# Kernel tuning notes

Hardware: AMD Instinct MI355X
Metric: run time of the kernel (lower is better)

## Reference

```python
import jax, jax.numpy as jnp
from jax import lax
import numpy as np

THRESHOLD = 0.9
KHALF = 5  # conv_kernel_size; full conv width = 2*KHALF + 1 = 11


def _cif_scan(eouts, alpha_norm, elens, ylens, Lp1):
    """Vectorized-over-batch integrate-and-fire scan over time (lax.scan)."""
    B, T, D = eouts.shape
    bidx = jnp.arange(B)
    dt = eouts.dtype

    def step(carry, xs):
        alpha_accum, state, n_tok, fired = carry
        a_t, e_t, t = xs  # a_t: [B], e_t: [B,D], t: scalar int
        alpha_accum = alpha_accum + a_t
        active = (t <= elens - 1) & (n_tok < ylens)
        fire = active & (alpha_accum >= THRESHOLD)
        ak1 = 1.0 - alpha_accum
        ak2 = a_t - ak1
        # attention-weight column for time t
        aw_col = jnp.zeros((B, Lp1), dt)
        w_old = jnp.where(fire, ak1, jnp.where(active, a_t, jnp.zeros((), dt)))
        aw_col = aw_col.at[bidx, n_tok].add(w_old)
        n_new = n_tok + fire.astype(n_tok.dtype)
        aw_col = aw_col.at[bidx, n_new].add(jnp.where(fire, ak2, jnp.zeros((), dt)))
        # fired output row (set once per token slot)
        fire_val = state + ak1[:, None] * e_t
        cur = fired[bidx, n_tok]
        fired = fired.at[bidx, n_tok].set(jnp.where(fire[:, None], fire_val, cur))
        # integrate / reset state
        state = jnp.where(fire[:, None], ak2[:, None] * e_t,
                          jnp.where(active[:, None], state + a_t[:, None] * e_t, state))
        alpha_accum = jnp.where(fire, ak2, alpha_accum)
        return (alpha_accum, state, n_new, fired), aw_col

    init = (jnp.zeros((B,), dt), jnp.zeros((B, D), dt),
            jnp.zeros((B,), jnp.int32), jnp.zeros((B, Lp1, D), dt))
    xs = (jnp.swapaxes(alpha_norm, 0, 1), jnp.swapaxes(eouts, 0, 1),
          jnp.arange(T))
    (_, _, _, fired), aw_cols = lax.scan(step, init, xs)
    aws = jnp.transpose(aw_cols, (1, 2, 0))[:, None]  # [B,1,Lp1,T]
    return fired, aws


def _forward(eouts, conv_w, conv_b, proj_w, proj_b, elens, ylens, L):
    # Conv1d over time, 'same' padding: [B,T,D] -> [B,T,C]
    conv_feat = lax.conv_general_dilated(
        eouts, conv_w, window_strides=(1,), padding=[(KHALF, KHALF)],
        dimension_numbers=('NWC', 'WIO', 'NWC')) + conv_b
    alpha = jax.nn.sigmoid(conv_feat @ proj_w + proj_b)[:, :, 0]  # [B,T]
    alpha_norm = alpha / jnp.sum(alpha, axis=1, keepdims=True) \
        * ylens[:, None].astype(alpha.dtype)
    fired, aws = _cif_scan(eouts, alpha_norm, elens, ylens, L + 1)
    return fired[:, :L], alpha, aws


def setup_inputs():
    key = jax.random.key(0)
    k1, k2, k3, k4, k5 = jax.random.split(key, 5)
    B, T, D, C = 16, 2048, 512, 512
    eouts = jax.random.normal(k1, (B, T, D), jnp.float32)
    elens = jnp.maximum(jax.random.randint(k2, (B,), 0, T), T // 2).astype(jnp.int32)
    ylens = jnp.maximum(jax.random.randint(k3, (B,), 0, 128), 32).astype(jnp.int32)
    conv_w = jax.random.normal(k4, (2 * KHALF + 1, D, C), jnp.float32) * 0.02
    conv_b = jnp.zeros((C,), jnp.float32)
    proj_w = jax.random.normal(k5, (C, 1), jnp.float32) * 0.05
    proj_b = jnp.zeros((1,), jnp.float32)
    return dict(eouts=eouts, conv_w=conv_w, conv_b=conv_b,
                proj_w=proj_w, proj_b=proj_b, elens=elens, ylens=ylens)


def reference(eouts, conv_w, conv_b, proj_w, proj_b, elens, ylens):
    L = int(jnp.max(ylens))  # max_len = ylens.max(), as in the original
    return _forward(eouts, conv_w, conv_b, proj_w, proj_b, elens, ylens, L)
```

## Files before the change

### kernel.cpp

```cpp
#include <hip/hip_runtime.h>
#include <math.h>

#define KHALF 5
#define MAXF 256

__global__ void k_weff(const float* __restrict__ conv_w, const float* __restrict__ conv_b,
                       const float* __restrict__ proj_w, const float* __restrict__ proj_b,
                       float* __restrict__ w_eff, float* __restrict__ b_eff,
                       int KD, int C) {
    int gid = blockIdx.x * blockDim.x + threadIdx.x;
    int wave = gid >> 6;
    int lane = gid & 63;
    if (wave > KD) return;
    float s = 0.f;
    if (wave < KD) {
        const float* row = conv_w + (size_t)wave * C;
        for (int c = lane * 4; c < C; c += 256) {
            float4 v = *reinterpret_cast<const float4*>(row + c);
            float4 w = *reinterpret_cast<const float4*>(proj_w + c);
            s += v.x * w.x + v.y * w.y + v.z * w.z + v.w * w.w;
        }
    } else {
        for (int c = lane; c < C; c += 64) s += conv_b[c] * proj_w[c];
    }
#pragma unroll
    for (int off = 32; off > 0; off >>= 1) s += __shfl_down(s, off, 64);
    if (lane == 0) {
        if (wave < KD) w_eff[wave] = s;
        else           b_eff[0] = s + proj_b[0];
    }
}

__global__ __launch_bounds__(256) void k_qdot(const float* __restrict__ eouts,
                                              const float* __restrict__ w_eff,
                                              float* __restrict__ q, int BT) {
    __shared__ float tile[64 * 68];
    __shared__ float wls[11 * 68];
    __shared__ float part[64 * 89];
    const int u0 = blockIdx.x * 64;
    const int rp = threadIdx.x & 31;
    const int s8 = threadIdx.x >> 5;
    float acc0[11], acc1[11];
#pragma unroll
    for (int k = 0; k < 11; ++k) { acc0[k] = 0.f; acc1[k] = 0.f; }
    for (int c = 0; c < 8; ++c) {
        __syncthreads();
#pragma unroll
        for (int it = 0; it < 4; ++it) {
            int idx = it * 256 + threadIdx.x;
            int r = idx >> 4, j4 = idx & 15;
            float4 v = *reinterpret_cast<const float4*>(
                eouts + (size_t)(u0 + r) * 512 + c * 64 + j4 * 4);
            *reinterpret_cast<float4*>(&tile[r * 68 + j4 * 4]) = v;
        }
        if (threadIdx.x < 176) {
            int k = threadIdx.x >> 4, sl = threadIdx.x & 15;
            float4 wv = *reinterpret_cast<const float4*>(
                w_eff + k * 512 + c * 64 + sl * 4);
            *reinterpret_cast<float4*>(&wls[k * 68 + sl * 4]) = wv;
        }
        __syncthreads();
#pragma unroll
        for (int j4 = 0; j4 < 2; ++j4) {
            const int dl = s8 * 8 + j4 * 4;
            float4 a0 = *reinterpret_cast<const float4*>(&tile[rp * 68 + dl]);
            float4 a1 = *reinterpret_cast<const float4*>(&tile[(rp + 32) * 68 + dl]);
#pragma unroll
            for (int k = 0; k < 11; ++k) {
                float4 wv = *reinterpret_cast<const float4*>(&wls[k * 68 + dl]);
                acc0[k] += a0.x * wv.x + a0.y * wv.y + a0.z * wv.z + a0.w * wv.w;
                acc1[k] += a1.x * wv.x + a1.y * wv.y + a1.z * wv.z + a1.w * wv.w;
            }
        }
    }
    __syncthreads();
#pragma unroll
    for (int k = 0; k < 11; ++k) {
        part[rp * 89 + s8 * 11 + k] = acc0[k];
        part[(rp + 32) * 89 + s8 * 11 + k] = acc1[k];
    }
    __syncthreads();
    if (threadIdx.x < 64) {
        int r = threadIdx.x;
        const float* p = &part[r * 89];
        float o[12];
#pragma unroll
        for (int k = 0; k < 11; ++k) {
            float s0 = (p[0 * 11 + k] + p[1 * 11 + k]) + (p[2 * 11 + k] + p[3 * 11 + k]);
            float s1 = (p[4 * 11 + k] + p[5 * 11 + k]) + (p[6 * 11 + k] + p[7 * 11 + k]);
            o[k] = s0 + s1;
        }
        o[11] = 0.f;
        float4* dst = reinterpret_cast<float4*>(q + (size_t)(u0 + r) * 12);
        dst[0] = make_float4(o[0], o[1], o[2], o[3]);
        dst[1] = make_float4(o[4], o[5], o[6], o[7]);
        dst[2] = make_float4(o[8], o[9], o[10], o[11]);
    }
}

__global__ __launch_bounds__(256) void k_sigpart(const float* __restrict__ q,
                                                 const float* __restrict__ b_eff,
                                                 float* __restrict__ alpha,
                                                 float* __restrict__ partials,
                                                 int T, int tcb) {
    __shared__ float qs[266 * 12];
    __shared__ float psm[4];
    int bx = blockIdx.x;
    int b = bx / tcb, tc = bx % tcb;
    int t0 = tc * 256;
    const float* qb = q + (size_t)b * T * 12;
    const int base = (t0 - 5) * 12;
    const int lim = T * 12;
    for (int i = threadIdx.x; i < 266 * 12; i += 256) {
        int gi = base + i;
        qs[i] = (gi >= 0 && gi < lim) ? qb[gi] : 0.f;
    }
    __syncthreads();
    int t = t0 + threadIdx.x;
    float sacc = b_eff[0];
#pragma unroll
    for (int k = 0; k < 11; ++k) sacc += qs[(threadIdx.x + k) * 12 + k];
    float al = 1.f / (1.f + expf(-sacc));
    alpha[(size_t)b * T + t] = al;
    float s = al;
    int lane = threadIdx.x & 63;
    int w = threadIdx.x >> 6;
#pragma unroll
    for (int off = 32; off > 0; off >>= 1) s += __shfl_down(s, off, 64);
    if (lane == 0) psm[w] = s;
    __syncthreads();
    if (threadIdx.x == 0) {
        float tot = 0.f;
        for (int i = 0; i < 4; ++i) tot += psm[i];
        partials[bx] = tot;
    }
}

__global__ void k_alpha(const float* __restrict__ eouts,
                        const float* __restrict__ w_eff,
                        const float* __restrict__ b_eff,
                        float* __restrict__ alpha,
                        int B, int T, int D) {
    const int W = 2 * KHALF + 1;
    int gid = blockIdx.x * blockDim.x + threadIdx.x;
    int wave = gid >> 6;
    int lane = gid & 63;
    if (wave >= B * T) return;
    int b = wave / T;
    int t = wave - b * T;
    int WD = W * D;
    int t0 = t - KHALF;
    float s = 0.f;
    if (t0 >= 0 && t0 + W <= T) {
        const float* base = eouts + ((size_t)b * T + t0) * D;
        for (int j = lane * 4; j < WD; j += 256) {
            float4 v = *reinterpret_cast<const float4*>(base + j);
            float4 w = *reinterpret_cast<const float4*>(w_eff + j);
            s += v.x * w.x + v.y * w.y + v.z * w.z + v.w * w.w;
        }
    } else {
        const float* base = eouts + (size_t)b * T * D;
        for (int j = lane; j < WD; j += 64) {
            int tt = t0 + j / D;
            if (tt >= 0 && tt < T) {
                int d = j - (j / D) * D;
                s += base[(size_t)tt * D + d] * w_eff[j];
            }
        }
    }
#pragma unroll
    for (int off = 32; off > 0; off >>= 1) s += __shfl_down(s, off, 64);
    if (lane == 0) {
        float logit = s + b_eff[0];
        alpha[(size_t)b * T + t] = 1.f / (1.f + expf(-logit));
    }
}

__global__ void k_chain(const float* __restrict__ alpha_in,
                        int use_part,
                        const float* __restrict__ partials, int npart,
                        const int* __restrict__ elens,
                        const int* __restrict__ ylens,
                        float* __restrict__ alpha_sum,
                        float* __restrict__ anorm,
                        int* __restrict__ n_fired,
                        int* __restrict__ fire_t,
                        float* __restrict__ fire_a1,
                        float* __restrict__ fire_a2,
                        int T, int Lp1) {
    extern __shared__ float an[];
    float* pf = an + T;
    __shared__ float sm[16];
    __shared__ float stot;
    int b = blockIdx.x;
    const float* row = alpha_in + (size_t)b * T;
    if ((T & 1023) == 0) {
        const float4* r4 = reinterpret_cast<const float4*>(row);
        float4* a4 = reinterpret_cast<float4*>(an);
        for (int i = threadIdx.x; i < (T >> 2); i += blockDim.x) a4[i] = r4[i];
    } else {
        for (int i = threadIdx.x; i < T; i += blockDim.x) an[i] = row[i];
    }
    __syncthreads();
    if (use_part) {
        if (threadIdx.x < npart && threadIdx.x < 16)
            sm[threadIdx.x] = partials[b * npart + threadIdx.x];
        __syncthreads();
        if (threadIdx.x == 0) {
            float tot = 0.f;
            if (npart <= 16) { for (int i = 0; i < npart; ++i) tot += sm[i]; }
            else { for (int i = 0; i < npart; ++i) tot += partials[b * npart + i]; }
            stot = tot;
            alpha_sum[b] = tot;
        }
    } else {
        float s = 0.f;
        for (int i = threadIdx.x; i < T; i += blockDim.x) s += an[i];
        int lane0 = threadIdx.x & 63;
        int w0 = threadIdx.x >> 6;
#pragma unroll
        for (int off = 32; off > 0; off >>= 1) s += __shfl_down(s, off, 64);
        if (lane0 == 0) sm[w0] = s;
        __syncthreads();
        if (threadIdx.x == 0) {
            float tot = 0.f;
            int nw = blockDim.x >> 6;
            for (int i = 0; i < nw; ++i) tot += sm[i];
            stot = tot;
            alpha_sum[b] = tot;
        }
    }
    __syncthreads();
    float ssum = stot;
    float yl = (float)ylens[b];
    float* __restrict__ anb = anorm + (size_t)b * T;
    for (int i = threadIdx.x; i < T; i += blockDim.x) {
        float v = an[i] / ssum * yl;
        an[i] = v;
        anb[i] = v;
    }
    __syncthreads();
    {
        int wv = threadIdx.x >> 6, ln = threadIdx.x & 63;
        int nchunks = (T + 63) >> 6;
        for (int c = wv; c < nchunks; c += 4) {
            int t = c * 64 + ln;
            float P = (t < T) ? an[t] : 0.f;
#pragma unroll
            for (int off = 1; off < 64; off <<= 1) {
                float tmp = __shfl_up(P, off, 64);
                if (ln >= off) P += tmp;
            }
            if (t < T) pf[t] = P;
        }
    }
    __syncthreads();
    if (threadIdx.x >= 64) return;
    int lane = threadIdx.x;
    int elen = elens[b];
    if (elen > T) elen = T;
    const int ylen = ylens[b];
    int* __restrict__ ft = fire_t + (size_t)b * Lp1;
    float* __restrict__ fa1 = fire_a1 + (size_t)b * Lp1;
    float* __restrict__ fa2 = fire_a2 + (size_t)b * Lp1;
    float accum = 0.f;
    int n = 0;
    bool done = false;
    for (int t0 = 0; t0 < elen && !done; t0 += 64) {
        int nv = elen - t0;
        if (nv > 64) nv = 64;
        float P = (t0 + lane < T) ? pf[t0 + lane] : 0.f;
        unsigned long long validmask = (nv == 64) ? ~0ull : ((1ull << nv) - 1ull);
        float base = accum;
        int start = 0;
        while (true) {
            bool cond = (base + P >= 0.9f);
            unsigned long long bal = __ballot(cond) & validmask;
            if (start > 0) bal &= (~0ull) << start;
            if (bal == 0) break;
            int u = __builtin_ctzll(bal);
            float Pu = pf[t0 + u];
            float au = an[t0 + u];
            float accum_f = base + Pu;
            float ak1 = 1.f - accum_f;
            float ak2 = au - ak1;
            if (lane == 0) { ft[n] = t0 + u; fa1[n] = ak1; fa2[n] = ak2; }
            ++n;
            if (n >= ylen) { done = true; break; }
            base = ak2 - Pu;
            start = u + 1;
            if (start >= nv) break;
        }
        if (!done) accum = base + pf[t0 + nv - 1];
    }
    if (lane == 0) n_fired[b] = n;
}

__global__ void k_awfired(const float* __restrict__ eouts,
                          const float* __restrict__ anorm,
                          const int* __restrict__ elens,
                          const int* __restrict__ ylens,
                          const int* __restrict__ n_fired,
                          const int* __restrict__ fire_t,
                          const float* __restrict__ fire_a1,
                          const float* __restrict__ fire_a2,
                          float* __restrict__ aws,
                          float* __restrict__ fired,
                          int T, int D, int L, int Lp1,
                          int AB, int tcpb, int DB) {
    if ((int)blockIdx.x < AB) {
        __shared__ int fts[MAXF];
        __shared__ float a1s[MAXF];
        __shared__ float a2s[MAXF];
        int b = blockIdx.x / tcpb;
        int tc = blockIdx.x % tcpb;
        int nf = n_fired[b];
        for (int i = threadIdx.x; i < nf; i += blockDim.x) {
            fts[i] = fire_t[(size_t)b * Lp1 + i];
            a1s[i] = fire_a1[(size_t)b * Lp1 + i];
            a2s[i] = fire_a2[(size_t)b * Lp1 + i];
        }
        __syncthreads();
        if (threadIdx.x >= 128) return;
        int t = tc * 128 + threadIdx.x;
        if (t >= T) return;
        int elen = elens[b];
        if (elen > T) elen = T;
        int ylen = ylens[b];
        bool active = (t < elen);
        int rowi = 0;
        bool isfire = false;
        float v1 = 0.f, v2 = 0.f;
        if (active) {
            int lo = 0, hi = nf;
            while (lo < hi) {
                int mid = (lo + hi) >> 1;
                if (fts[mid] < t) lo = mid + 1; else hi = mid;
            }
            rowi = lo;
            isfire = (rowi < nf && fts[rowi] == t);
            if (isfire) { v1 = a1s[rowi]; v2 = a2s[rowi]; }
            else if (rowi < ylen) v1 = anorm[(size_t)b * T + t];
            else active = false;
        }
        float* col = aws + (size_t)b * Lp1 * T + t;
        for (int r = 0; r < Lp1; ++r) {
            float v = 0.f;
            if (active) {
                if (r == rowi) v = v1;
                else if (isfire && r == rowi + 1) v = v2;
            }
            col[(size_t)r * T] = v;
        }
    } else {
        int idx = blockIdx.x - AB;
        int b = idx / (L * DB);
        int rem = idx % (L * DB);
        int n = rem / DB;
        int d = (rem % DB) * 256 + threadIdx.x;
        if (d >= D) return;
        int nf = n_fired[b];
        float* dst = fired + ((size_t)b * L + n) * D + d;
        if (n >= nf) { *dst = 0.f; return; }
        int t0 = (n == 0) ? 0 : fire_t[(size_t)b * Lp1 + n - 1];
        int t1 = fire_t[(size_t)b * Lp1 + n];
        float ak1 = fire_a1[(size_t)b * Lp1 + n];
        float ak2p = (n > 0) ? fire_a2[(size_t)b * Lp1 + n - 1] : 0.f;
        const float* an_g = anorm + (size_t)b * T;
        const float* e = eouts + ((size_t)b * T + t0) * D + d;
        float accv;
        if (t1 == t0) {
            accv = ak1 * e[0];
        } else {
            float w0 = (n > 0) ? ak2p : an_g[t0];
            accv = w0 * e[0];
            float a0 = 0.f, a1 = 0.f, a2 = 0.f, a3 = 0.f;
            int t = t0 + 1;
            const float* ee = e + D;
            for (; t + 3 < t1; t += 4, ee += 4 * (size_t)D) {
                a0 += an_g[t]     * ee[0];
                a1 += an_g[t + 1] * ee[D];
                a2 += an_g[t + 2] * ee[2 * (size_t)D];
                a3 += an_g[t + 3] * ee[3 * (size_t)D];
            }
            for (; t < t1; ++t, ee += D) a0 += an_g[t] * ee[0];
            accv += ((a0 + a1) + (a2 + a3));
            accv += ak1 * ee[0];
        }
        *dst = accv;
    }
}

extern "C" void kernel_launch(void* const* d_in, const int* in_sizes, int n_in,
                              void* d_out, int out_size, void* d_ws, size_t ws_size,
                              hipStream_t stream) {
    const float* eouts  = (const float*)d_in[0];
    const float* conv_w = (const float*)d_in[1];
    const float* conv_b = (const float*)d_in[2];
    const float* proj_w = (const float*)d_in[3];
    const float* proj_b = (const float*)d_in[4];
    const int*   elens  = (const int*)d_in[5];
    const int*   ylens  = (const int*)d_in[6];

    const int B = in_sizes[5];
    const int C = in_sizes[2];
    const int W = 2 * KHALF + 1;
    const int D = in_sizes[1] / (W * C);
    const int T = in_sizes[0] / (B * D);
    const int L = (out_size - 2 * B * T) / (B * (D + T));
    const int Lp1 = L + 1;
    const int BT = B * T;
    const int tcb = (T + 255) / 256;

    float* out   = (float*)d_out;
    float* fired = out;
    float* alpha = out + (size_t)B * L * D;
    float* aws   = alpha + (size_t)B * T;

    char*  ws        = (char*)d_ws;
    float* w_eff     = (float*)ws;
    float* b_eff     = (float*)(ws + (size_t)W * D * 4);
    float* alpha_sum = b_eff + 16;
    int*   n_fired   = (int*)(alpha_sum + B + 16);
    int*   fire_t    = n_fired + B + 16;
    float* fire_a1   = (float*)(fire_t + (size_t)B * Lp1 + 16);
    float* fire_a2   = fire_a1 + (size_t)B * Lp1 + 16;
    float* anorm     = fire_a2 + (size_t)B * Lp1 + 16;
    float* qbuf      = anorm + (size_t)B * T + 16;
    float* partials  = qbuf + (size_t)BT * 12 + 16;
    size_t ws_need   = (size_t)((char*)(partials + (size_t)B * tcb + 16) - ws);

    const int KD = W * D;
    {
        long long threads = (long long)(KD + 1) * 64;
        int blocks = (int)((threads + 255) / 256);
        k_weff<<<blocks, 256, 0, stream>>>(conv_w, conv_b, proj_w, proj_b,
                                           w_eff, b_eff, KD, C);
    }

    const bool fast = (ws_size >= ws_need) && (D == 512) && (C == 512) &&
                      (BT % 64 == 0) && (T % 256 == 0) && (T <= 16384) &&
                      (Lp1 <= MAXF);
    if (fast) {
        k_qdot<<<BT / 64, 256, 0, stream>>>(eouts, w_eff, qbuf, BT);
        k_sigpart<<<B * tcb, 256, 0, stream>>>(qbuf, b_eff, alpha, partials, T, tcb);
    } else {
        long long threads = (long long)BT * 64;
        int blocks = (int)((threads + 255) / 256);
        k_alpha<<<blocks, 256, 0, stream>>>(eouts, w_eff, b_eff, alpha, B, T, D);
    }

    k_chain<<<B, 256, 2 * T * sizeof(float), stream>>>(
        alpha, fast ? 1 : 0, partials, tcb,
        elens, ylens, alpha_sum, anorm,
        n_fired, fire_t, fire_a1, fire_a2, T, Lp1);

    {
        int tcpb = (T + 127) / 128;
        int AB = B * tcpb;
        int DB = (D + 255) / 256;
        int FB = B * L * DB;
        k_awfired<<<AB + FB, 256, 0, stream>>>(eouts, anorm,
                                               elens, ylens, n_fired,
                                               fire_t, fire_a1, fire_a2,
                                               aws, fired, T, D, L, Lp1,
                                               AB, tcpb, DB);
    }
}
```

Baseline: 163.6 us.

## Fuse sigmoid into chain kernel, prezero aws in prep, vectorize fired rows

The sigmoid/partial-sum kernel is folded into k_chain, so each batch block computes alpha in 256-step chunks and the partials buffer and one launch go away. Zeroing of the large aws output moves into the weight-prep kernel as extra fill blocks. The aws writer then stores only the nonzero entries per column, and the fired-row path uses float4 loads with two token rows per block. The fused chain now does the alpha work on only B blocks, which serialises it, and the sparse aws writes depend on the fill kernel running first on the same stream.

New measurement: 189.5 us. +15.8%, slower.

```diff
diff --git a/kernel.cpp b/kernel.cpp
--- a/kernel.cpp
+++ b/kernel.cpp
@@ -4,10 +4,22 @@
 #define KHALF 5
 #define MAXF 256
 
-__global__ void k_weff(const float* __restrict__ conv_w, const float* __restrict__ conv_b,
+__global__ void k_prep(const float* __restrict__ conv_w, const float* __restrict__ conv_b,
                        const float* __restrict__ proj_w, const float* __restrict__ proj_b,
                        float* __restrict__ w_eff, float* __restrict__ b_eff,
-                       int KD, int C) {
+                       int KD, int C,
+                       float* __restrict__ aws, long long awsN, int WB, int NFILL) {
+    if ((int)blockIdx.x >= WB) {
+        long long N4 = awsN >> 2;
+        long long gid = (long long)(blockIdx.x - WB) * 256 + threadIdx.x;
+        float4 z = make_float4(0.f, 0.f, 0.f, 0.f);
+        float4* a4 = reinterpret_cast<float4*>(aws);
+        long long stride = (long long)NFILL * 256;
+        for (long long i = gid; i < N4; i += stride) a4[i] = z;
+        int tail = (int)(awsN & 3);
+        if (gid < tail) aws[4 * N4 + gid] = 0.f;
+        return;
+    }
     int gid = blockIdx.x * blockDim.x + threadIdx.x;
     int wave = gid >> 6;
     int lane = gid & 63;
@@ -95,44 +107,6 @@
         dst[0] = make_float4(o[0], o[1], o[2], o[3]);
         dst[1] = make_float4(o[4], o[5], o[6], o[7]);
         dst[2] = make_float4(o[8], o[9], o[10], o[11]);
-    }
-}
-
-__global__ __launch_bounds__(256) void k_sigpart(const float* __restrict__ q,
-                                                 const float* __restrict__ b_eff,
-                                                 float* __restrict__ alpha,
-                                                 float* __restrict__ partials,
-                                                 int T, int tcb) {
-    __shared__ float qs[266 * 12];
-    __shared__ float psm[4];
-    int bx = blockIdx.x;
-    int b = bx / tcb, tc = bx % tcb;
-    int t0 = tc * 256;
-    const float* qb = q + (size_t)b * T * 12;
-    const int base = (t0 - 5) * 12;
-    const int lim = T * 12;
-    for (int i = threadIdx.x; i < 266 * 12; i += 256) {
-        int gi = base + i;
-        qs[i] = (gi >= 0 && gi < lim) ? qb[gi] : 0.f;
-    }
-    __syncthreads();
-    int t = t0 + threadIdx.x;
-    float sacc = b_eff[0];
-#pragma unroll
-    for (int k = 0; k < 11; ++k) sacc += qs[(threadIdx.x + k) * 12 + k];
-    float al = 1.f / (1.f + expf(-sacc));
-    alpha[(size_t)b * T + t] = al;
-    float s = al;
-    int lane = threadIdx.x & 63;
-    int w = threadIdx.x >> 6;
-#pragma unroll
-    for (int off = 32; off > 0; off >>= 1) s += __shfl_down(s, off, 64);
-    if (lane == 0) psm[w] = s;
-    __syncthreads();
-    if (threadIdx.x == 0) {
-        float tot = 0.f;
-        for (int i = 0; i < 4; ++i) tot += psm[i];
-        partials[bx] = tot;
     }
 }
 
@@ -177,11 +151,12 @@
 }
 
 __global__ void k_chain(const float* __restrict__ alpha_in,
-                        int use_part,
-                        const float* __restrict__ partials, int npart,
+                        const float* __restrict__ qbuf,
+                        const float* __restrict__ b_eff,
+                        int fused,
                         const int* __restrict__ elens,
                         const int* __restrict__ ylens,
-                        float* __restrict__ alpha_sum,
+                        float* __restrict__ alpha_out,
                         float* __restrict__ anorm,
                         int* __restrict__ n_fired,
                         int* __restrict__ fire_t,
@@ -190,30 +165,54 @@
                         int T, int Lp1) {
     extern __shared__ float an[];
     float* pf = an + T;
-    __shared__ float sm[16];
+    __shared__ float qs[266 * 12];
+    __shared__ float sm[64];
     __shared__ float stot;
     int b = blockIdx.x;
-    const float* row = alpha_in + (size_t)b * T;
-    if ((T & 1023) == 0) {
-        const float4* r4 = reinterpret_cast<const float4*>(row);
-        float4* a4 = reinterpret_cast<float4*>(an);
-        for (int i = threadIdx.x; i < (T >> 2); i += blockDim.x) a4[i] = r4[i];
-    } else {
-        for (int i = threadIdx.x; i < T; i += blockDim.x) an[i] = row[i];
-    }
-    __syncthreads();
-    if (use_part) {
-        if (threadIdx.x < npart && threadIdx.x < 16)
-            sm[threadIdx.x] = partials[b * npart + threadIdx.x];
+    if (fused) {
+        const float* qb = qbuf + (size_t)b * T * 12;
+        const int lim = T * 12;
+        const int nchunks = T >> 8;
+        const float be = b_eff[0];
+        for (int c = 0; c < nchunks; ++c) {
+            __syncthreads();
+            int t0 = c * 256;
+            int base = (t0 - 5) * 12;
+            for (int i = threadIdx.x; i < 266 * 12; i += 256) {
+                int gi = base + i;
+                qs[i] = (gi >= 0 && gi < lim) ? qb[gi] : 0.f;
+            }
+            __syncthreads();
+            int t = t0 + threadIdx.x;
+            float sacc = be;
+#pragma unroll
+            for (int k = 0; k < 11; ++k) sacc += qs[(threadIdx.x + k) * 12 + k];
+            float al = 1.f / (1.f + expf(-sacc));
+            an[t] = al;
+            alpha_out[(size_t)b * T + t] = al;
+            float s = al;
+            int lane = threadIdx.x & 63;
+            int w = threadIdx.x >> 6;
+#pragma unroll
+            for (int off = 32; off > 0; off >>= 1) s += __shfl_down(s, off, 64);
+            if (lane == 0) sm[c * 4 + w] = s;
+        }
         __syncthreads();
         if (threadIdx.x == 0) {
             float tot = 0.f;
-            if (npart <= 16) { for (int i = 0; i < npart; ++i) tot += sm[i]; }
-            else { for (int i = 0; i < npart; ++i) tot += partials[b * npart + i]; }
+            for (int c = 0; c < nchunks; ++c) {
+                float pc = sm[c * 4];
+                pc += sm[c * 4 + 1];
+                pc += sm[c * 4 + 2];
+                pc += sm[c * 4 + 3];
+                tot += pc;
+            }
             stot = tot;
-            alpha_sum[b] = tot;
         }
     } else {
+        const float* row = alpha_in + (size_t)b * T;
+        for (int i = threadIdx.x; i < T; i += blockDim.x) an[i] = row[i];
+        __syncthreads();
         float s = 0.f;
         for (int i = threadIdx.x; i < T; i += blockDim.x) s += an[i];
         int lane0 = threadIdx.x & 63;
@@ -227,7 +226,6 @@
             int nw = blockDim.x >> 6;
             for (int i = 0; i < nw; ++i) tot += sm[i];
             stot = tot;
-            alpha_sum[b] = tot;
         }
     }
     __syncthreads();
@@ -307,7 +305,7 @@
                           float* __restrict__ aws,
                           float* __restrict__ fired,
                           int T, int D, int L, int Lp1,
-                          int AB, int tcpb, int DB) {
+                          int AB, int tcpb, int nLh) {
     if ((int)blockIdx.x < AB) {
         __shared__ int fts[MAXF];
         __shared__ float a1s[MAXF];
@@ -321,73 +319,125 @@
             a2s[i] = fire_a2[(size_t)b * Lp1 + i];
         }
         __syncthreads();
-        if (threadIdx.x >= 128) return;
-        int t = tc * 128 + threadIdx.x;
+        int t = tc * 256 + threadIdx.x;
         if (t >= T) return;
         int elen = elens[b];
         if (elen > T) elen = T;
         int ylen = ylens[b];
-        bool active = (t < elen);
-        int rowi = 0;
-        bool isfire = false;
-        float v1 = 0.f, v2 = 0.f;
-        if (active) {
-            int lo = 0, hi = nf;
-            while (lo < hi) {
-                int mid = (lo + hi) >> 1;
-                if (fts[mid] < t) lo = mid + 1; else hi = mid;
-            }
-            rowi = lo;
-            isfire = (rowi < nf && fts[rowi] == t);
-            if (isfire) { v1 = a1s[rowi]; v2 = a2s[rowi]; }
-            else if (rowi < ylen) v1 = anorm[(size_t)b * T + t];
-            else active = false;
-        }
+        if (t >= elen) return;
+        int lo = 0, hi = nf;
+        while (lo < hi) {
+            int mid = (lo + hi) >> 1;
+            if (fts[mid] < t) lo = mid + 1; else hi = mid;
+        }
+        int rowi = lo;
+        bool isfire = (rowi < nf && fts[rowi] == t);
         float* col = aws + (size_t)b * Lp1 * T + t;
-        for (int r = 0; r < Lp1; ++r) {
-            float v = 0.f;
-            if (active) {
-                if (r == rowi) v = v1;
-                else if (isfire && r == rowi + 1) v = v2;
-            }
-            col[(size_t)r * T] = v;
+        if (isfire) {
+            col[(size_t)rowi * T] = a1s[rowi];
+            col[(size_t)(rowi + 1) * T] = a2s[rowi];
+        } else if (rowi < ylen) {
+            col[(size_t)rowi * T] = anorm[(size_t)b * T + t];
         }
     } else {
         int idx = blockIdx.x - AB;
-        int b = idx / (L * DB);
-        int rem = idx % (L * DB);
-        int n = rem / DB;
-        int d = (rem % DB) * 256 + threadIdx.x;
-        if (d >= D) return;
+        int b = idx / nLh;
+        int j = idx % nLh;
+        int half = threadIdx.x >> 7;
+        int dl = threadIdx.x & 127;
+        int n = 2 * j + half;
+        if (n >= L) return;
         int nf = n_fired[b];
-        float* dst = fired + ((size_t)b * L + n) * D + d;
-        if (n >= nf) { *dst = 0.f; return; }
-        int t0 = (n == 0) ? 0 : fire_t[(size_t)b * Lp1 + n - 1];
-        int t1 = fire_t[(size_t)b * Lp1 + n];
-        float ak1 = fire_a1[(size_t)b * Lp1 + n];
-        float ak2p = (n > 0) ? fire_a2[(size_t)b * Lp1 + n - 1] : 0.f;
-        const float* an_g = anorm + (size_t)b * T;
-        const float* e = eouts + ((size_t)b * T + t0) * D + d;
-        float accv;
-        if (t1 == t0) {
-            accv = ak1 * e[0];
+        if ((D & 3) == 0) {
+            int D4 = D >> 2;
+            float4* dst = reinterpret_cast<float4*>(fired + ((size_t)b * L + n) * D);
+            if (n >= nf) {
+                for (int d4 = dl; d4 < D4; d4 += 128)
+                    dst[d4] = make_float4(0.f, 0.f, 0.f, 0.f);
+                return;
+            }
+            int t0 = (n == 0) ? 0 : fire_t[(size_t)b * Lp1 + n - 1];
+            int t1 = fire_t[(size_t)b * Lp1 + n];
+            float ak1 = fire_a1[(size_t)b * Lp1 + n];
+            float ak2p = (n > 0) ? fire_a2[(size_t)b * Lp1 + n - 1] : 0.f;
+            const float* an_g = anorm + (size_t)b * T;
+            const float4* ebase = reinterpret_cast<const float4*>(
+                eouts + ((size_t)b * T + t0) * D);
+            for (int d4 = dl; d4 < D4; d4 += 128) {
+                const float4* e = ebase + d4;
+                float4 accv;
+                if (t1 == t0) {
+                    float4 v = e[0];
+                    accv.x = ak1 * v.x; accv.y = ak1 * v.y;
+                    accv.z = ak1 * v.z; accv.w = ak1 * v.w;
+                } else {
+                    float w0 = (n > 0) ? ak2p : an_g[t0];
+                    float4 v = e[0];
+                    accv.x = w0 * v.x; accv.y = w0 * v.y;
+                    accv.z = w0 * v.z; accv.w = w0 * v.w;
+                    float4 a0 = make_float4(0.f, 0.f, 0.f, 0.f);
+                    float4 a1 = a0, a2 = a0, a3 = a0;
+                    int t = t0 + 1;
+                    const float4* ee = e + D4;
+                    for (; t + 3 < t1; t += 4, ee += 4 * (size_t)D4) {
+                        float wa = an_g[t], wb = an_g[t + 1];
+                        float wc = an_g[t + 2], wd = an_g[t + 3];
+                        float4 va = ee[0], vb = ee[D4], vc = ee[2 * (size_t)D4], vd = ee[3 * (size_t)D4];
+                        a0.x += wa * va.x; a0.y += wa * va.y; a0.z += wa * va.z; a0.w += wa * va.w;
+                        a1.x += wb * vb.x; a1.y += wb * vb.y; a1.z += wb * vb.z; a1.w += wb * vb.w;
+                        a2.x += wc * vc.x; a2.y += wc * vc.y; a2.z += wc * vc.z; a2.w += wc * vc.w;
+                        a3.x += wd * vd.x; a3.y += wd * vd.y; a3.z += wd * vd.z; a3.w += wd * vd.w;
+                    }
+                    for (; t < t1; ++t, ee += D4) {
+                        float wa = an_g[t];
+                        float4 va = ee[0];
+                        a0.x += wa * va.x; a0.y += wa * va.y; a0.z += wa * va.z; a0.w += wa * va.w;
+                    }
+                    accv.x += ((a0.x + a1.x) + (a2.x + a3.x));
+                    accv.y += ((a0.y + a1.y) + (a2.y + a3.y));
+                    accv.z += ((a0.z + a1.z) + (a2.z + a3.z));
+                    accv.w += ((a0.w + a1.w) + (a2.w + a3.w));
+                    float4 vl = ee[0];
+                    accv.x += ak1 * vl.x; accv.y += ak1 * vl.y;
+                    accv.z += ak1 * vl.z; accv.w += ak1 * vl.w;
+                }
+                dst[d4] = accv;
+            }
         } else {
-            float w0 = (n > 0) ? ak2p : an_g[t0];
-            accv = w0 * e[0];
-            float a0 = 0.f, a1 = 0.f, a2 = 0.f, a3 = 0.f;
-            int t = t0 + 1;
-            const float* ee = e + D;
-            for (; t + 3 < t1; t += 4, ee += 4 * (size_t)D) {
-                a0 += an_g[t]     * ee[0];
-                a1 += an_g[t + 1] * ee[D];
-                a2 += an_g[t + 2] * ee[2 * (size_t)D];
-                a3 += an_g[t + 3] * ee[3 * (size_t)D];
-            }
-            for (; t < t1; ++t, ee += D) a0 += an_g[t] * ee[0];
-            accv += ((a0 + a1) + (a2 + a3));
-            accv += ak1 * ee[0];
-        }
-        *dst = accv;
+            float* dst = fired + ((size_t)b * L + n) * D;
+            if (n >= nf) {
+                for (int d = dl; d < D; d += 128) dst[d] = 0.f;
+                return;
+            }
+            int t0 = (n == 0) ? 0 : fire_t[(size_t)b * Lp1 + n - 1];
+            int t1 = fire_t[(size_t)b * Lp1 + n];
+            float ak1 = fire_a1[(size_t)b * Lp1 + n];
+            float ak2p = (n > 0) ? fire_a2[(size_t)b * Lp1 + n - 1] : 0.f;
+            const float* an_g = anorm + (size_t)b * T;
+            for (int d = dl; d < D; d += 128) {
+                const float* e = eouts + ((size_t)b * T + t0) * D + d;
+                float accv;
+                if (t1 == t0) {
+                    accv = ak1 * e[0];
+                } else {
+                    float w0 = (n > 0) ? ak2p : an_g[t0];
+                    accv = w0 * e[0];
+                    float a0 = 0.f, a1 = 0.f, a2 = 0.f, a3 = 0.f;
+                    int t = t0 + 1;
+                    const float* ee = e + D;
+                    for (; t + 3 < t1; t += 4, ee += 4 * (size_t)D) {
+                        a0 += an_g[t]     * ee[0];
+                        a1 += an_g[t + 1] * ee[D];
+                        a2 += an_g[t + 2] * ee[2 * (size_t)D];
+                        a3 += an_g[t + 3] * ee[3 * (size_t)D];
+                    }
+                    for (; t < t1; ++t, ee += D) a0 += an_g[t] * ee[0];
+                    accv += ((a0 + a1) + (a2 + a3));
+                    accv += ak1 * ee[0];
+                }
+                dst[d] = accv;
+            }
+        }
     }
 }
 
@@ -410,7 +460,6 @@
     const int L = (out_size - 2 * B * T) / (B * (D + T));
     const int Lp1 = L + 1;
     const int BT = B * T;
-    const int tcb = (T + 255) / 256;
 
     float* out   = (float*)d_out;
     float* fired = out;
@@ -420,22 +469,23 @@
     char*  ws        = (char*)d_ws;
     float* w_eff     = (float*)ws;
     float* b_eff     = (float*)(ws + (size_t)W * D * 4);
-    float* alpha_sum = b_eff + 16;
-    int*   n_fired   = (int*)(alpha_sum + B + 16);
+    int*   n_fired   = (int*)(b_eff + 16);
     int*   fire_t    = n_fired + B + 16;
     float* fire_a1   = (float*)(fire_t + (size_t)B * Lp1 + 16);
     float* fire_a2   = fire_a1 + (size_t)B * Lp1 + 16;
     float* anorm     = fire_a2 + (size_t)B * Lp1 + 16;
     float* qbuf      = anorm + (size_t)B * T + 16;
-    float* partials  = qbuf + (size_t)BT * 12 + 16;
-    size_t ws_need   = (size_t)((char*)(partials + (size_t)B * tcb + 16) - ws);
+    size_t ws_need   = (size_t)((char*)(qbuf + (size_t)BT * 12 + 16) - ws);
 
     const int KD = W * D;
     {
-        long long threads = (long long)(KD + 1) * 64;
-        int blocks = (int)((threads + 255) / 256);
-        k_weff<<<blocks, 256, 0, stream>>>(conv_w, conv_b, proj_w, proj_b,
-                                           w_eff, b_eff, KD, C);
+        long long wthreads = (long long)(KD + 1) * 64;
+        int WB = (int)((wthreads + 255) / 256);
+        int NFILL = 2048;
+        long long awsN = (long long)B * Lp1 * T;
+        k_prep<<<WB + NFILL, 256, 0, stream>>>(conv_w, conv_b, proj_w, proj_b,
+                                               w_eff, b_eff, KD, C,
+                                               aws, awsN, WB, NFILL);
     }
 
     const bool fast = (ws_size >= ws_need) && (D == 512) && (C == 512) &&
@@ -443,27 +493,30 @@
                       (Lp1 <= MAXF);
     if (fast) {
         k_qdot<<<BT / 64, 256, 0, stream>>>(eouts, w_eff, qbuf, BT);
-        k_sigpart<<<B * tcb, 256, 0, stream>>>(qbuf, b_eff, alpha, partials, T, tcb);
+        k_chain<<<B, 256, 2 * T * sizeof(float), stream>>>(
+            nullptr, qbuf, b_eff, 1,
+            elens, ylens, alpha, anorm,
+            n_fired, fire_t, fire_a1, fire_a2, T, Lp1);
     } else {
         long long threads = (long long)BT * 64;
         int blocks = (int)((threads + 255) / 256);
         k_alpha<<<blocks, 256, 0, stream>>>(eouts, w_eff, b_eff, alpha, B, T, D);
-    }
-
-    k_chain<<<B, 256, 2 * T * sizeof(float), stream>>>(
-        alpha, fast ? 1 : 0, partials, tcb,
-        elens, ylens, alpha_sum, anorm,
-        n_fired, fire_t, fire_a1, fire_a2, T, Lp1);
+        k_chain<<<B, 256, 2 * T * sizeof(float), stream>>>(
+            alpha, nullptr, nullptr, 0,
+            elens, ylens, alpha, anorm,
+            n_fired, fire_t, fire_a1, fire_a2, T, Lp1);
+    }
 
     {
-        int tcpb = (T + 127) / 128;
+        int tcpb = (T + 255) / 256;
         int AB = B * tcpb;
-        int DB = (D + 255) / 256;
-        int FB = B * L * DB;
+        int nLh = (L + 1) / 2;
+        if (nLh < 1) nLh = 1;
+        int FB = B * nLh;
         k_awfired<<<AB + FB, 256, 0, stream>>>(eouts, anorm,
                                                elens, ylens, n_fired,
                                                fire_t, fire_a1, fire_a2,
                                                aws, fired, T, D, L, Lp1,
-                                               AB, tcpb, DB);
+                                               AB, tcpb, nLh);
     }
 }
```
